# Kernel tuning notes

Measured on AMD Instinct MI355X. Metric: run time of the kernel, lower is better.

Reference implementation:

```python
import jax, jax.numpy as jnp
import numpy as np

N = 50000
DIM = 768   # input_dim == feature dim (self.L)
D_ATT = 128 # self.D


def setup_inputs() -> dict:
    key = jax.random.key(0)
    ks = jax.random.split(key, 6)
    s = lambda fan_in: 1.0 / np.sqrt(fan_in)
    return {
        "x": jax.random.normal(ks[0], (1, N, DIM), dtype=jnp.float32),
        "W_feat": jax.random.normal(ks[1], (DIM, DIM), dtype=jnp.float32) * s(DIM),
        "b_feat": jax.random.normal(ks[2], (DIM,), dtype=jnp.float32) * s(DIM),
        "W_a": jax.random.normal(ks[3], (D_ATT, DIM), dtype=jnp.float32) * s(DIM),
        "W_b": jax.random.normal(ks[4], (D_ATT, DIM), dtype=jnp.float32) * s(DIM),
        "W_c": jax.random.normal(ks[5], (1, D_ATT), dtype=jnp.float32) * s(D_ATT),
    }


def reference(x, W_feat, b_feat, W_a, W_b, W_c):
    # x: [1, N, DIM] -> squeeze bag dim -> [N, DIM]
    h = jax.nn.relu(jnp.einsum('nd,ed->ne', x[0], W_feat) + b_feat)  # [N, 768]
    a = jax.nn.relu(jnp.einsum('nd,kd->nk', h, W_a))      # [N, 128]
    b = jax.nn.sigmoid(jnp.einsum('nd,kd->nk', h, W_b))   # [N, 128]
    logits = jnp.einsum('nk,ok->on', a * b, W_c)           # [1, N] (transpose fused)
    A = jax.nn.softmax(logits, axis=-1)                    # [1, N]
    return jnp.einsum('on,nd->od', A, h)                   # [1, 768]
```

## Files before the change

kernel.cpp:

```cpp
#include <hip/hip_runtime.h>
#include <hip/hip_bf16.h>
#include <stdint.h>

#define DEVINL __device__ __forceinline__

using bf16x8 = __attribute__((ext_vector_type(8))) short;
using f32x4  = __attribute__((ext_vector_type(4))) float;

static constexpr int NPTS = 50000;
static constexpr int NPAD = 50176;
static constexpr int DIM  = 768;
static constexpr int DATT = 128;
static constexpr int NRB  = NPAD / 128;

DEVINL ushort f2b(float f) {
  uint32_t u = __float_as_uint(f);
  u += 0x7fffu + ((u >> 16) & 1u);
  return (ushort)(u >> 16);
}
DEVINL float b2f(ushort u) { return __uint_as_float(((uint32_t)u) << 16); }

DEVINL void gload_lds16(const void* g, void* l) {
  __builtin_amdgcn_global_load_lds((const __attribute__((address_space(1))) void*)g,
                                   (__attribute__((address_space(3))) void*)l,
                                   16, 0, 0);
}

__global__ void cvt8_kernel(const float* __restrict__ src, ushort* __restrict__ dst,
                            int n8_src, int n8_dst) {
  const int stride = gridDim.x * blockDim.x;
  for (int i = blockIdx.x * blockDim.x + threadIdx.x; i < n8_dst; i += stride) {
    float4 v0 = {0.f, 0.f, 0.f, 0.f}, v1 = {0.f, 0.f, 0.f, 0.f};
    if (i < n8_src) {
      const float4* s4 = (const float4*)src;
      v0 = s4[(long)i * 2];
      v1 = s4[(long)i * 2 + 1];
    }
    ushort4 o0 = { f2b(v0.x), f2b(v0.y), f2b(v0.z), f2b(v0.w) };
    ushort4 o1 = { f2b(v1.x), f2b(v1.y), f2b(v1.z), f2b(v1.w) };
    ((ushort4*)dst)[(long)i * 2]     = o0;
    ((ushort4*)dst)[(long)i * 2 + 1] = o1;
  }
}

__global__ void cvt_weights_kernel(const float* __restrict__ Wf, const float* __restrict__ Wa,
                                   const float* __restrict__ Wb,
                                   ushort* __restrict__ wfb, ushort* __restrict__ wab,
                                   ushort* __restrict__ wbb) {
  const int NF = DIM * DIM / 8, NA = DATT * DIM / 8;
  int i = blockIdx.x * blockDim.x + threadIdx.x;
  const float* src; ushort* dst; int j;
  if (i < NF)               { src = Wf; dst = wfb; j = i; }
  else if (i < NF + NA)     { src = Wa; dst = wab; j = i - NF; }
  else if (i < NF + 2 * NA) { src = Wb; dst = wbb; j = i - NF - NA; }
  else return;
  const float4* s4 = (const float4*)src;
  float4 v0 = s4[(long)j * 2];
  float4 v1 = s4[(long)j * 2 + 1];
  ushort4 o0 = { f2b(v0.x), f2b(v0.y), f2b(v0.z), f2b(v0.w) };
  ushort4 o1 = { f2b(v1.x), f2b(v1.y), f2b(v1.z), f2b(v1.w) };
  ((ushort4*)dst)[(long)j * 2]     = o0;
  ((ushort4*)dst)[(long)j * 2 + 1] = o1;
}

__global__ __launch_bounds__(512)
void gemm_h_kernel(const ushort* __restrict__ A, const ushort* __restrict__ B,
                   const float* __restrict__ bias, ushort* __restrict__ H) {
  __shared__ ushort lds[3][24576];

  const int tid  = threadIdx.x;
  const int wid  = tid >> 6;
  const int lane = tid & 63;

  const int bid  = blockIdx.x;
  const int wgid = (bid & 7) * 147 + (bid >> 3);
  const int row0 = (wgid / 6) * 256;
  const int col0 = (wgid % 6) * 128;

  const int wrow = (wid >> 1) * 64;
  const int wcol = (wid & 1) * 64;

  const int srow = lane >> 3;
  const int scol = ((lane & 7) ^ (lane >> 3)) * 8;

  const ushort* Abase = A + (long)row0 * DIM;
  const ushort* Bbase = B + (long)col0 * DIM;

  auto stage = [&](int t, int buf) {
    const int k0 = t * 64;
#pragma unroll
    for (int i = 0; i < 4; ++i) {
      const int ch = i * 8 + wid;
      gload_lds16(Abase + (long)(ch * 8 + srow) * DIM + k0 + scol,
                  &lds[buf][ch * 512]);
    }
#pragma unroll
    for (int i = 0; i < 2; ++i) {
      const int ch = i * 8 + wid;
      gload_lds16(Bbase + (long)(ch * 8 + srow) * DIM + k0 + scol,
                  &lds[buf][16384 + ch * 512]);
    }
  };

  f32x4 acc[4][4] = {};

  stage(0, 0);
  stage(1, 1);
  int c = 0;
  for (int t = 0; t < 12; ++t) {
    if (t < 10) {
      const int nb = (c == 0) ? 2 : c - 1;
      stage(t + 2, nb);
      asm volatile("s_waitcnt vmcnt(12)" ::: "memory");
    } else if (t == 10) {
      asm volatile("s_waitcnt vmcnt(6)" ::: "memory");
    } else {
      asm volatile("s_waitcnt vmcnt(0)" ::: "memory");
    }
    __builtin_amdgcn_s_barrier();
    __builtin_amdgcn_sched_barrier(0);

    const ushort* Ab = &lds[c][0];
    const ushort* Bb = &lds[c][16384];
#pragma unroll
    for (int kk = 0; kk < 2; ++kk) {
      const int j = kk * 4 + (lane >> 4);
      bf16x8 a[4];
#pragma unroll
      for (int m = 0; m < 4; ++m) {
        const int ra = wrow + m * 16 + (lane & 15);
        a[m] = *(const bf16x8*)(Ab + ra * 64 + ((j ^ (ra & 7)) << 3));
      }
#pragma unroll
      for (int n = 0; n < 4; ++n) {
        const int rb = wcol + n * 16 + (lane & 15);
        bf16x8 b = *(const bf16x8*)(Bb + rb * 64 + ((j ^ (rb & 7)) << 3));
#pragma unroll
        for (int m = 0; m < 4; ++m)
          acc[m][n] = __builtin_amdgcn_mfma_f32_16x16x32_bf16(a[m], b, acc[m][n], 0, 0, 0);
      }
    }
    __builtin_amdgcn_sched_barrier(0);
    __builtin_amdgcn_s_barrier();
    c = (c == 2) ? 0 : c + 1;
  }

  const int lq = lane >> 4;
  const int lc = lane & 15;
#pragma unroll
  for (int n = 0; n < 4; ++n) {
    const int cg = col0 + wcol + n * 16 + lc;
    const float bv = bias[cg];
#pragma unroll
    for (int m = 0; m < 4; ++m) {
      const int rg = row0 + wrow + m * 16 + lq * 4;
#pragma unroll
      for (int r2 = 0; r2 < 4; ++r2) {
        float v = acc[m][n][r2] + bv;
        v = fmaxf(v, 0.0f);
        H[(long)(rg + r2) * DIM + cg] = f2b(v);
      }
    }
  }
}

__global__ __launch_bounds__(512)
void gate_kernel(const ushort* __restrict__ Hm, const ushort* __restrict__ Wa,
                 const ushort* __restrict__ Wb, const float* __restrict__ Wc,
                 float* __restrict__ logits) {
  __shared__ ushort Hs [128 * 64];
  __shared__ ushort Was[128 * 64];
  __shared__ ushort Wbs[128 * 64];
  const int tid  = threadIdx.x;
  const int wid  = tid >> 6;
  const int lane = tid & 63;
  const int row0 = blockIdx.x * 128;

  f32x4 fa[8] = {};
  f32x4 fb[8] = {};

  const int ld_r = lane >> 3;
  const int ld_c = (lane & 7) * 8;

  for (int k0 = 0; k0 < DIM; k0 += 64) {
    __syncthreads();
#pragma unroll
    for (int i = 0; i < 2; ++i) {
      const int ch = i * 8 + wid;
      const int r  = ch * 8 + ld_r;
      gload_lds16(Hm + (long)(row0 + r) * DIM + k0 + ld_c, Hs  + ch * 512);
      gload_lds16(Wa + (long)r * DIM        + k0 + ld_c, Was + ch * 512);
      gload_lds16(Wb + (long)r * DIM        + k0 + ld_c, Wbs + ch * 512);
    }
    __syncthreads();
#pragma unroll
    for (int kk = 0; kk < 2; ++kk) {
      const int kc = kk * 32 + (lane >> 4) * 8;
      bf16x8 h = *(const bf16x8*)(Hs + (wid * 16 + (lane & 15)) * 64 + kc);
#pragma unroll
      for (int n = 0; n < 8; ++n) {
        bf16x8 wa = *(const bf16x8*)(Was + (n * 16 + (lane & 15)) * 64 + kc);
        bf16x8 wb = *(const bf16x8*)(Wbs + (n * 16 + (lane & 15)) * 64 + kc);
        fa[n] = __builtin_amdgcn_mfma_f32_16x16x32_bf16(h, wa, fa[n], 0, 0, 0);
        fb[n] = __builtin_amdgcn_mfma_f32_16x16x32_bf16(h, wb, fb[n], 0, 0, 0);
      }
    }
  }

  const int lc = lane & 15;
  const int lq = lane >> 4;
  float g[4];
#pragma unroll
  for (int r = 0; r < 4; ++r) {
    float s = 0.f;
#pragma unroll
    for (int n = 0; n < 8; ++n) {
      float av = fmaxf(fa[n][r], 0.f);
      float sg = 1.f / (1.f + expf(-fb[n][r]));
      s += av * sg * Wc[n * 16 + lc];
    }
    s += __shfl_xor(s, 1);
    s += __shfl_xor(s, 2);
    s += __shfl_xor(s, 4);
    s += __shfl_xor(s, 8);
    g[r] = s;
  }
  if (lc == 0) {
    const int rbase = row0 + wid * 16 + lq * 4;
#pragma unroll
    for (int r = 0; r < 4; ++r) {
      const int nidx = rbase + r;
      if (nidx < NPTS) logits[nidx] = g[r];
    }
  }
}

__global__ __launch_bounds__(1024)
void softmax_stats_kernel(const float* __restrict__ logits, float* __restrict__ stats) {
  __shared__ float red[1024];
  const int tid = threadIdx.x;
  float m = -1e30f;
  for (int i = tid; i < NPTS; i += 1024) m = fmaxf(m, logits[i]);
  red[tid] = m; __syncthreads();
  for (int s = 512; s > 0; s >>= 1) {
    if (tid < s) red[tid] = fmaxf(red[tid], red[tid + s]);
    __syncthreads();
  }
  m = red[0];
  __syncthreads();
  float sum = 0.f;
  for (int i = tid; i < NPTS; i += 1024) sum += expf(logits[i] - m);
  red[tid] = sum; __syncthreads();
  for (int s = 512; s > 0; s >>= 1) {
    if (tid < s) red[tid] += red[tid + s];
    __syncthreads();
  }
  if (tid == 0) { stats[0] = m; stats[1] = red[0]; }
}

__global__ __launch_bounds__(192)
void weighted_partial_kernel(const ushort* __restrict__ Hm, const float* __restrict__ logits,
                             const float* __restrict__ stats, float* __restrict__ part) {
  __shared__ float w[128];
  const int b = blockIdx.x, tid = threadIdx.x;
  const int n0 = b * 128;
  if (tid < 128) {
    const int n = n0 + tid;
    w[tid] = (n < NPTS) ? expf(logits[n] - stats[0]) : 0.f;
  }
  __syncthreads();
  float4 acc = {0.f, 0.f, 0.f, 0.f};
  const ushort* hp = Hm + (long)n0 * DIM + tid * 4;
#pragma unroll 4
  for (int r = 0; r < 128; ++r) {
    const float wr = w[r];
    ushort4 v = *(const ushort4*)(hp + (long)r * DIM);
    acc.x += wr * b2f(v.x);
    acc.y += wr * b2f(v.y);
    acc.z += wr * b2f(v.z);
    acc.w += wr * b2f(v.w);
  }
  ((float4*)(part + (long)b * DIM))[tid] = acc;
}

__global__ void final_reduce_kernel(const float* __restrict__ part,
                                    const float* __restrict__ stats,
                                    float* __restrict__ out) {
  const int c = blockIdx.x * blockDim.x + threadIdx.x;
  if (c >= DIM) return;
  float s = 0.f;
  for (int b = 0; b < NRB; ++b) s += part[(long)b * DIM + c];
  out[c] = s / stats[1];
}

extern "C" void kernel_launch(void* const* d_in, const int* in_sizes, int n_in,
                              void* d_out, int out_size, void* d_ws, size_t ws_size,
                              hipStream_t stream) {
  const float* x  = (const float*)d_in[0];
  const float* Wf = (const float*)d_in[1];
  const float* bf = (const float*)d_in[2];
  const float* Wa = (const float*)d_in[3];
  const float* Wb = (const float*)d_in[4];
  const float* Wc = (const float*)d_in[5];
  float* out = (float*)d_out;

  char* p = (char*)d_ws;
  ushort* xb  = (ushort*)p; p += (size_t)NPAD * DIM * 2;
  ushort* hb  = (ushort*)p; p += (size_t)NPAD * DIM * 2;
  ushort* wfb = (ushort*)p; p += (size_t)DIM * DIM * 2;
  ushort* wab = (ushort*)p; p += (size_t)DATT * DIM * 2;
  ushort* wbb = (ushort*)p; p += (size_t)DATT * DIM * 2;
  float* logits = (float*)p; p += (size_t)NPAD * 4;
  float* stats  = (float*)p; p += 256;
  float* part   = (float*)p; p += (size_t)NRB * DIM * 4;

  cvt8_kernel<<<2048, 256, 0, stream>>>(x, xb, NPTS * DIM / 8, NPAD * DIM / 8);
  cvt_weights_kernel<<<384, 256, 0, stream>>>(Wf, Wa, Wb, wfb, wab, wbb);

  gemm_h_kernel<<<196 * 6, 512, 0, stream>>>(xb, wfb, bf, hb);
  gate_kernel<<<NRB, 512, 0, stream>>>(hb, wab, wbb, Wc, logits);
  softmax_stats_kernel<<<1, 1024, 0, stream>>>(logits, stats);
  weighted_partial_kernel<<<NRB, 192, 0, stream>>>(hb, logits, stats, part);
  final_reduce_kernel<<<3, 256, 0, stream>>>(part, stats, out);
}
```

Baseline: 225.7 us.

## Merge conversion kernels, split GEMM staging per half-K, parallelize softmax stats

The x and weight bf16 conversions now run in one launch. The GEMM main loop is split into two half-K phases: A-tile and B-tile global-to-LDS loads are issued separately between LDS fragment reads and MFMA blocks, and the MFMA blocks run at raised wave priority. This is meant to overlap loads with matrix math more finely. The softmax statistics move from a single 1024-thread block to 49 blocks plus a one-wave combine kernel, removing a serial reduction over 50k logits at the cost of one extra launch.

```diff
diff --git a/kernel.cpp b/kernel.cpp
--- a/kernel.cpp
+++ b/kernel.cpp
@@ -12,6 +12,7 @@
 static constexpr int DIM  = 768;
 static constexpr int DATT = 128;
 static constexpr int NRB  = NPAD / 128;
+static constexpr int NSMB = 49;
 
 DEVINL ushort f2b(float f) {
   uint32_t u = __float_as_uint(f);
@@ -26,41 +27,31 @@
                                    16, 0, 0);
 }
 
-__global__ void cvt8_kernel(const float* __restrict__ src, ushort* __restrict__ dst,
-                            int n8_src, int n8_dst) {
+__global__ void cvt_all_kernel(const float* __restrict__ x, const float* __restrict__ Wf,
+                               const float* __restrict__ Wa, const float* __restrict__ Wb,
+                               ushort* __restrict__ xb, ushort* __restrict__ wfb,
+                               ushort* __restrict__ wab, ushort* __restrict__ wbb) {
+  const int NX8 = NPAD * DIM / 8, NXS = NPTS * DIM / 8;
+  const int NF = DIM * DIM / 8, NA = DATT * DIM / 8;
+  const int total = NX8 + NF + 2 * NA;
   const int stride = gridDim.x * blockDim.x;
-  for (int i = blockIdx.x * blockDim.x + threadIdx.x; i < n8_dst; i += stride) {
-    float4 v0 = {0.f, 0.f, 0.f, 0.f}, v1 = {0.f, 0.f, 0.f, 0.f};
-    if (i < n8_src) {
+  for (int i = blockIdx.x * blockDim.x + threadIdx.x; i < total; i += stride) {
+    const float* src; ushort* dst; int j; bool zero = false;
+    if (i < NX8)                { src = x;  dst = xb;  j = i; zero = (i >= NXS); }
+    else if (i < NX8 + NF)      { src = Wf; dst = wfb; j = i - NX8; }
+    else if (i < NX8 + NF + NA) { src = Wa; dst = wab; j = i - NX8 - NF; }
+    else                        { src = Wb; dst = wbb; j = i - NX8 - NF - NA; }
+    float4 v0 = {0.f,0.f,0.f,0.f}, v1 = {0.f,0.f,0.f,0.f};
+    if (!zero) {
       const float4* s4 = (const float4*)src;
-      v0 = s4[(long)i * 2];
-      v1 = s4[(long)i * 2 + 1];
+      v0 = s4[(long)j * 2];
+      v1 = s4[(long)j * 2 + 1];
     }
     ushort4 o0 = { f2b(v0.x), f2b(v0.y), f2b(v0.z), f2b(v0.w) };
     ushort4 o1 = { f2b(v1.x), f2b(v1.y), f2b(v1.z), f2b(v1.w) };
-    ((ushort4*)dst)[(long)i * 2]     = o0;
-    ((ushort4*)dst)[(long)i * 2 + 1] = o1;
-  }
-}
-
-__global__ void cvt_weights_kernel(const float* __restrict__ Wf, const float* __restrict__ Wa,
-                                   const float* __restrict__ Wb,
-                                   ushort* __restrict__ wfb, ushort* __restrict__ wab,
-                                   ushort* __restrict__ wbb) {
-  const int NF = DIM * DIM / 8, NA = DATT * DIM / 8;
-  int i = blockIdx.x * blockDim.x + threadIdx.x;
-  const float* src; ushort* dst; int j;
-  if (i < NF)               { src = Wf; dst = wfb; j = i; }
-  else if (i < NF + NA)     { src = Wa; dst = wab; j = i - NF; }
-  else if (i < NF + 2 * NA) { src = Wb; dst = wbb; j = i - NF - NA; }
-  else return;
-  const float4* s4 = (const float4*)src;
-  float4 v0 = s4[(long)j * 2];
-  float4 v1 = s4[(long)j * 2 + 1];
-  ushort4 o0 = { f2b(v0.x), f2b(v0.y), f2b(v0.z), f2b(v0.w) };
-  ushort4 o1 = { f2b(v1.x), f2b(v1.y), f2b(v1.z), f2b(v1.w) };
-  ((ushort4*)dst)[(long)j * 2]     = o0;
-  ((ushort4*)dst)[(long)j * 2 + 1] = o1;
+    ((ushort4*)dst)[(long)j * 2]     = o0;
+    ((ushort4*)dst)[(long)j * 2 + 1] = o1;
+  }
 }
 
 __global__ __launch_bounds__(512)
@@ -86,7 +77,7 @@
   const ushort* Abase = A + (long)row0 * DIM;
   const ushort* Bbase = B + (long)col0 * DIM;
 
-  auto stage = [&](int t, int buf) {
+  auto STAGE_A = [&](int t, int buf) {
     const int k0 = t * 64;
 #pragma unroll
     for (int i = 0; i < 4; ++i) {
@@ -94,6 +85,9 @@
       gload_lds16(Abase + (long)(ch * 8 + srow) * DIM + k0 + scol,
                   &lds[buf][ch * 512]);
     }
+  };
+  auto STAGE_B = [&](int t, int buf) {
+    const int k0 = t * 64;
 #pragma unroll
     for (int i = 0; i < 2; ++i) {
       const int ch = i * 8 + wid;
@@ -104,28 +98,21 @@
 
   f32x4 acc[4][4] = {};
 
-  stage(0, 0);
-  stage(1, 1);
+  STAGE_A(0, 0); STAGE_B(0, 0);
+  STAGE_A(1, 1); STAGE_B(1, 1);
+  asm volatile("s_waitcnt vmcnt(6)" ::: "memory");
+  __builtin_amdgcn_s_barrier();
+
   int c = 0;
+#pragma unroll 1
   for (int t = 0; t < 12; ++t) {
-    if (t < 10) {
-      const int nb = (c == 0) ? 2 : c - 1;
-      stage(t + 2, nb);
-      asm volatile("s_waitcnt vmcnt(12)" ::: "memory");
-    } else if (t == 10) {
-      asm volatile("s_waitcnt vmcnt(6)" ::: "memory");
-    } else {
-      asm volatile("s_waitcnt vmcnt(0)" ::: "memory");
-    }
-    __builtin_amdgcn_s_barrier();
-    __builtin_amdgcn_sched_barrier(0);
-
+    const int nb = (c == 0) ? 2 : c - 1;
     const ushort* Ab = &lds[c][0];
     const ushort* Bb = &lds[c][16384];
-#pragma unroll
-    for (int kk = 0; kk < 2; ++kk) {
-      const int j = kk * 4 + (lane >> 4);
-      bf16x8 a[4];
+
+    {
+      const int j = lane >> 4;
+      bf16x8 a[4], b[4];
 #pragma unroll
       for (int m = 0; m < 4; ++m) {
         const int ra = wrow + m * 16 + (lane & 15);
@@ -134,14 +121,54 @@
 #pragma unroll
       for (int n = 0; n < 4; ++n) {
         const int rb = wcol + n * 16 + (lane & 15);
-        bf16x8 b = *(const bf16x8*)(Bb + rb * 64 + ((j ^ (rb & 7)) << 3));
+        b[n] = *(const bf16x8*)(Bb + rb * 64 + ((j ^ (rb & 7)) << 3));
+      }
+      if (t < 10) STAGE_A(t + 2, nb);
+      __builtin_amdgcn_s_barrier();
+      asm volatile("s_waitcnt lgkmcnt(0)" ::: "memory");
+      __builtin_amdgcn_sched_barrier(0);
+      __builtin_amdgcn_s_setprio(1);
+#pragma unroll
+      for (int n = 0; n < 4; ++n)
 #pragma unroll
         for (int m = 0; m < 4; ++m)
-          acc[m][n] = __builtin_amdgcn_mfma_f32_16x16x32_bf16(a[m], b, acc[m][n], 0, 0, 0);
-      }
-    }
-    __builtin_amdgcn_sched_barrier(0);
-    __builtin_amdgcn_s_barrier();
+          acc[m][n] = __builtin_amdgcn_mfma_f32_16x16x32_bf16(a[m], b[n], acc[m][n], 0, 0, 0);
+      __builtin_amdgcn_s_setprio(0);
+      __builtin_amdgcn_sched_barrier(0);
+      __builtin_amdgcn_s_barrier();
+    }
+    {
+      const int j = 4 + (lane >> 4);
+      bf16x8 a[4], b[4];
+#pragma unroll
+      for (int m = 0; m < 4; ++m) {
+        const int ra = wrow + m * 16 + (lane & 15);
+        a[m] = *(const bf16x8*)(Ab + ra * 64 + ((j ^ (ra & 7)) << 3));
+      }
+#pragma unroll
+      for (int n = 0; n < 4; ++n) {
+        const int rb = wcol + n * 16 + (lane & 15);
+        b[n] = *(const bf16x8*)(Bb + rb * 64 + ((j ^ (rb & 7)) << 3));
+      }
+      if (t < 10) STAGE_B(t + 2, nb);
+      if (t < 10) {
+        asm volatile("s_waitcnt vmcnt(6)" ::: "memory");
+      } else if (t == 10) {
+        asm volatile("s_waitcnt vmcnt(0)" ::: "memory");
+      }
+      __builtin_amdgcn_s_barrier();
+      asm volatile("s_waitcnt lgkmcnt(0)" ::: "memory");
+      __builtin_amdgcn_sched_barrier(0);
+      __builtin_amdgcn_s_setprio(1);
+#pragma unroll
+      for (int n = 0; n < 4; ++n)
+#pragma unroll
+        for (int m = 0; m < 4; ++m)
+          acc[m][n] = __builtin_amdgcn_mfma_f32_16x16x32_bf16(a[m], b[n], acc[m][n], 0, 0, 0);
+      __builtin_amdgcn_s_setprio(0);
+      __builtin_amdgcn_sched_barrier(0);
+      __builtin_amdgcn_s_barrier();
+    }
     c = (c == 2) ? 0 : c + 1;
   }
 
@@ -236,26 +263,37 @@
 }
 
 __global__ __launch_bounds__(1024)
-void softmax_stats_kernel(const float* __restrict__ logits, float* __restrict__ stats) {
+void softmax_part_kernel(const float* __restrict__ logits, float* __restrict__ part2) {
   __shared__ float red[1024];
   const int tid = threadIdx.x;
-  float m = -1e30f;
-  for (int i = tid; i < NPTS; i += 1024) m = fmaxf(m, logits[i]);
-  red[tid] = m; __syncthreads();
+  const int n = blockIdx.x * 1024 + tid;
+  const float v = (n < NPTS) ? logits[n] : -1e30f;
+  red[tid] = v; __syncthreads();
   for (int s = 512; s > 0; s >>= 1) {
     if (tid < s) red[tid] = fmaxf(red[tid], red[tid + s]);
     __syncthreads();
   }
-  m = red[0];
+  const float m = red[0];
   __syncthreads();
-  float sum = 0.f;
-  for (int i = tid; i < NPTS; i += 1024) sum += expf(logits[i] - m);
-  red[tid] = sum; __syncthreads();
+  red[tid] = (n < NPTS) ? expf(v - m) : 0.f;
+  __syncthreads();
   for (int s = 512; s > 0; s >>= 1) {
     if (tid < s) red[tid] += red[tid + s];
     __syncthreads();
   }
-  if (tid == 0) { stats[0] = m; stats[1] = red[0]; }
+  if (tid == 0) { part2[blockIdx.x * 2] = m; part2[blockIdx.x * 2 + 1] = red[0]; }
+}
+
+__global__ void softmax_comb_kernel(const float* __restrict__ part2,
+                                    float* __restrict__ stats) {
+  const int l = threadIdx.x;
+  float m = (l < NSMB) ? part2[l * 2]     : -1e30f;
+  float s = (l < NSMB) ? part2[l * 2 + 1] : 0.f;
+  float M = m;
+  for (int o = 32; o > 0; o >>= 1) M = fmaxf(M, __shfl_xor(M, o));
+  float sc = s * expf(m - M);
+  for (int o = 32; o > 0; o >>= 1) sc += __shfl_xor(sc, o);
+  if (l == 0) { stats[0] = M; stats[1] = sc; }
 }
 
 __global__ __launch_bounds__(192)
@@ -312,14 +350,15 @@
   ushort* wbb = (ushort*)p; p += (size_t)DATT * DIM * 2;
   float* logits = (float*)p; p += (size_t)NPAD * 4;
   float* stats  = (float*)p; p += 256;
+  float* part2  = (float*)p; p += 1024;
   float* part   = (float*)p; p += (size_t)NRB * DIM * 4;
 
-  cvt8_kernel<<<2048, 256, 0, stream>>>(x, xb, NPTS * DIM / 8, NPAD * DIM / 8);
-  cvt_weights_kernel<<<384, 256, 0, stream>>>(Wf, Wa, Wb, wfb, wab, wbb);
+  cvt_all_kernel<<<2048, 256, 0, stream>>>(x, Wf, Wa, Wb, xb, wfb, wab, wbb);
 
   gemm_h_kernel<<<196 * 6, 512, 0, stream>>>(xb, wfb, bf, hb);
   gate_kernel<<<NRB, 512, 0, stream>>>(hb, wab, wbb, Wc, logits);
-  softmax_stats_kernel<<<1, 1024, 0, stream>>>(logits, stats);
+  softmax_part_kernel<<<NSMB, 1024, 0, stream>>>(logits, part2);
+  softmax_comb_kernel<<<1, 64, 0, stream>>>(part2, stats);
   weighted_partial_kernel<<<NRB, 192, 0, stream>>>(hb, logits, stats, part);
   final_reduce_kernel<<<3, 256, 0, stream>>>(part, stats, out);
 }
```

Measured after the change: 219.1 us. -2.9%, faster.
